# Kernel tuning notes

Hardware: AMD Instinct MI355X
Metric: run time of the kernel (lower is better)

## Reference

```python
import jax, jax.numpy as jnp
import numpy as np

B, IN, OUT = 4096, 1024, 1024


def setup_inputs() -> dict:
    key = jax.random.key(0)
    ks = jax.random.split(key, 11)
    xav = 1.0 / np.sqrt(IN + OUT)  # Xavier-style scale for sigmoid/tanh layers
    d = {
        "x": jax.random.normal(ks[0], (B, IN), dtype=jnp.float32),
        "h": jax.random.normal(ks[1], (B, OUT), dtype=jnp.float32),
        "c": jax.random.normal(ks[2], (B, OUT), dtype=jnp.float32),
        "w_f": jax.random.normal(ks[3], (IN + OUT, OUT), dtype=jnp.float32) * xav,
        "b_f": jnp.zeros((1, OUT), dtype=jnp.float32),
        "w_i": jax.random.normal(ks[4], (IN + OUT, OUT), dtype=jnp.float32) * xav,
        "b_i": jnp.zeros((1, OUT), dtype=jnp.float32),
        "w_c": jax.random.normal(ks[5], (IN + OUT, OUT), dtype=jnp.float32) * xav,
        "b_c": jnp.zeros((1, OUT), dtype=jnp.float32),
        "w_o": jax.random.normal(ks[6], (IN + OUT, OUT), dtype=jnp.float32) * xav,
        "b_o": jnp.zeros((1, OUT), dtype=jnp.float32),
    }
    return d


def reference(x, h, c, w_f, b_f, w_i, b_i, w_c, b_c, w_o, b_o):
    # combined input [B, IN+OUT]
    z = jnp.concatenate([x, h], axis=1)
    f = jax.nn.sigmoid(z @ w_f + b_f)      # forget gate
    i = jax.nn.sigmoid(z @ w_i + b_i)      # update (input) gate
    g = jnp.tanh(z @ w_c + b_c)            # candidate cell
    o = jax.nn.sigmoid(z @ w_o + b_o)      # output gate
    c_new = c * f + i * g
    h_new = jnp.tanh(c_new) * o
    return h_new
```

## Files before the change

### kernel.cpp

```cpp
#include <hip/hip_runtime.h>
#include <hip/hip_bf16.h>

typedef short short8 __attribute__((ext_vector_type(8)));
typedef float f32x4 __attribute__((ext_vector_type(4)));

#define NB 4096
#define KZ 2048
#define NG 1024
#define NKS 32

__device__ __forceinline__ unsigned short f2bf(float f) {
  unsigned int u = __float_as_uint(f);
  u += 0x7FFFu + ((u >> 16) & 1u);
  return (unsigned short)(u >> 16);
}
__device__ __forceinline__ float bf2f(unsigned short s) {
  return __uint_as_float(((unsigned int)s) << 16);
}
__device__ __forceinline__ void gload_lds16(const void* g, void* l) {
  __builtin_amdgcn_global_load_lds(
      (__attribute__((address_space(1))) void*)g,
      (__attribute__((address_space(3))) void*)l, 16, 0, 0);
}
__device__ __forceinline__ float sigm(float x) { return 1.f / (1.f + __expf(-x)); }
__device__ __forceinline__ float tanh_fast(float x) {
  float e = __expf(-2.f * fabsf(x));
  float r = (1.f - e) / (1.f + e);
  return copysignf(r, x);
}

__global__ void zsplit_kernel(const float* __restrict__ x, const float* __restrict__ h,
                              unsigned short* __restrict__ zh) {
  int idx = blockIdx.x * 256 + threadIdx.x;
  int e = idx << 2;
  int r = e >> 11;
  int k = e & (KZ - 1);
  const float* src = (k < 1024) ? (x + ((size_t)r << 10) + k)
                                : (h + ((size_t)r << 10) + (k - 1024));
  float4 v = *reinterpret_cast<const float4*>(src);
  float vf[4] = {v.x, v.y, v.z, v.w};
  unsigned short hh[4];
#pragma unroll
  for (int j = 0; j < 4; ++j) hh[j] = f2bf(vf[j]);
  uint2 H = make_uint2((unsigned)hh[0] | ((unsigned)hh[1] << 16),
                       (unsigned)hh[2] | ((unsigned)hh[3] << 16));
  *reinterpret_cast<uint2*>(zh + e) = H;
}

__global__ void wsplit_kernel(const float* __restrict__ w0, const float* __restrict__ w1,
                              const float* __restrict__ w2, const float* __restrict__ w3,
                              unsigned short* __restrict__ wh, unsigned short* __restrict__ wl) {
  __shared__ float tile[32][33];
  int g = blockIdx.z;
  const float* w = (g == 0) ? w0 : (g == 1) ? w1 : (g == 2) ? w2 : w3;
  int k0 = blockIdx.x << 5;
  int n0 = blockIdx.y << 5;
  int t = threadIdx.x;
  int rk = t >> 3, q = t & 7;
  float4 v = *reinterpret_cast<const float4*>(w + (size_t)(k0 + rk) * NG + n0 + (q << 2));
  tile[rk][(q << 2) + 0] = v.x;
  tile[rk][(q << 2) + 1] = v.y;
  tile[rk][(q << 2) + 2] = v.z;
  tile[rk][(q << 2) + 3] = v.w;
  __syncthreads();
  int n = t >> 3, kq = t & 7;
  unsigned short hs[4], ls[4];
#pragma unroll
  for (int j = 0; j < 4; ++j) {
    float f = tile[(kq << 2) + j][n];
    unsigned short hi = f2bf(f);
    unsigned short lo = f2bf(f - bf2f(hi));
    hs[j] = hi; ls[j] = lo;
  }
  int nn = n0 + n;
  int p = ((nn >> 6) << 8) | (((nn >> 4) & 3) << 6) | (g << 4) | (nn & 15);
  size_t o = (size_t)p * KZ + k0 + (kq << 2);
  uint2 H = make_uint2((unsigned)hs[0] | ((unsigned)hs[1] << 16),
                       (unsigned)hs[2] | ((unsigned)hs[3] << 16));
  uint2 L = make_uint2((unsigned)ls[0] | ((unsigned)ls[1] << 16),
                       (unsigned)ls[2] | ((unsigned)ls[3] << 16));
  *reinterpret_cast<uint2*>(wh + o) = H;
  *reinterpret_cast<uint2*>(wl + o) = L;
}

#define MFMA(a, b, c) __builtin_amdgcn_mfma_f32_16x16x32_bf16((a), (b), (c), 0, 0, 0)
#define ABAR() asm volatile("s_barrier" ::: "memory")
#define LGKM(N) asm volatile("s_waitcnt lgkmcnt(" #N ")" ::: "memory")
#define VMC0() asm volatile("s_waitcnt vmcnt(0)" ::: "memory")
#define SB() __builtin_amdgcn_sched_barrier(0)
#define PRIO1() __builtin_amdgcn_s_setprio(1)
#define PRIO0() __builtin_amdgcn_s_setprio(0)

__global__ __launch_bounds__(512, 2) void lstm_gemm256_kernel(
    const unsigned short* __restrict__ zh,
    const unsigned short* __restrict__ wh, const unsigned short* __restrict__ wl,
    const float* __restrict__ c_in, const float* __restrict__ bf_,
    const float* __restrict__ bi_, const float* __restrict__ bc_,
    const float* __restrict__ bo_, float* __restrict__ out) {
  __shared__ unsigned short As[2 * 16384];
  __shared__ unsigned short Bh[16384];
  __shared__ unsigned short Bl[16384];
  const int t = threadIdx.x;
  const int lane = t & 63;
  const int wid = t >> 6;
  const int wr = wid >> 2;
  const int wc = wid & 3;
  const int l15 = lane & 15;
  const int l4 = lane >> 4;

  const int bid = blockIdx.x;
  const int swz = ((bid & 7) << 5) + (bid >> 3);
  const int bx = swz & 15;
  const int by = swz >> 4;
  const int brow0 = by << 8;
  const int pcol0 = bx << 8;

  char* AsB = (char*)As;
  char* BhB = (char*)Bh;
  char* BlB = (char*)Bl;

  int aoff[2], boff[2];
#pragma unroll
  for (int j = 0; j < 2; ++j) {
    int row = (j << 6) + (t >> 3);
    int sl = (t & 7) ^ (row & 7);
    aoff[j] = (brow0 + row) * KZ + (sl << 3);
    boff[j] = (pcol0 + row) * KZ + (sl << 3);
  }
  const int ldsw = wid << 10;

  auto STAGE = [&](int s, int hx) {
    if (s >= NKS) return;
    const int kk = s << 6;
    if (hx < 2) {
      const int lb = ((s & 1) << 15) + (hx << 14);
#pragma unroll
      for (int j = 0; j < 2; ++j)
        gload_lds16(zh + aoff[j] + hx * (128 * KZ) + kk, AsB + lb + (j << 13) + ldsw);
    } else if (hx < 4) {
      const int hq = hx - 2;
#pragma unroll
      for (int j = 0; j < 2; ++j)
        gload_lds16(wh + boff[j] + hq * (128 * KZ) + kk, BhB + (hq << 14) + (j << 13) + ldsw);
    } else {
      const int hq = hx - 4;
#pragma unroll
      for (int j = 0; j < 2; ++j)
        gload_lds16(wl + boff[j] + hq * (128 * KZ) + kk, BlB + (hq << 14) + (j << 13) + ldsw);
    }
  };

  f32x4 acc[8][4];
#pragma unroll
  for (int m = 0; m < 8; ++m)
#pragma unroll
    for (int n = 0; n < 4; ++n) acc[m][n] = (f32x4){0.f, 0.f, 0.f, 0.f};

  const int rx = l15 & 7;
  const int sx0 = (l4 ^ rx) << 4;
  const int sx1 = ((4 + l4) ^ rx) << 4;
  const int aB = l15 << 7;
  const int bB = ((wc & 1) << 13) + (l15 << 7);
  const int aW = wr << 14;
  const int bW = (wc >> 1) << 14;

  short8 aL0[4], aH0[4], aL1[4], aH1[4], vbh0[4], vbh1[4], vbl0[4], vbl1[4];

  STAGE(0, 0); STAGE(0, 1); STAGE(0, 2); STAGE(0, 3); STAGE(0, 4); STAGE(0, 5);
  VMC0();
  ABAR();

  for (int ks = 0; ks < NKS; ++ks) {
    const int abase = ((ks & 1) << 15) + aW;

#pragma unroll
    for (int m = 0; m < 4; ++m)
      aL0[m] = *reinterpret_cast<const short8*>(AsB + abase + aB + (m << 11) + sx0);
#pragma unroll
    for (int n = 0; n < 4; ++n)
      vbh0[n] = *reinterpret_cast<const short8*>(BhB + bW + bB + (n << 11) + sx0);
    SB();
#pragma unroll
    for (int n = 0; n < 4; ++n)
      vbl0[n] = *reinterpret_cast<const short8*>(BlB + bW + bB + (n << 11) + sx0);
    SB();
    STAGE(ks + 1, 0);
    LGKM(4); SB();
    PRIO1();
#pragma unroll
    for (int m = 0; m < 4; ++m)
#pragma unroll
      for (int n = 0; n < 4; ++n) acc[m][n] = MFMA(aL0[m], vbh0[n], acc[m][n]);
    PRIO0();

#pragma unroll
    for (int m = 0; m < 4; ++m)
      aH0[m] = *reinterpret_cast<const short8*>(AsB + abase + aB + ((m + 4) << 11) + sx0);
    SB();
    STAGE(ks + 1, 1);
    LGKM(4); SB();
    PRIO1();
#pragma unroll
    for (int m = 0; m < 4; ++m)
#pragma unroll
      for (int n = 0; n < 4; ++n) acc[m][n] = MFMA(aL0[m], vbl0[n], acc[m][n]);
    PRIO0();

#pragma unroll
    for (int m = 0; m < 4; ++m)
      aL1[m] = *reinterpret_cast<const short8*>(AsB + abase + aB + (m << 11) + sx1);
#pragma unroll
    for (int n = 0; n < 4; ++n)
      vbh1[n] = *reinterpret_cast<const short8*>(BhB + bW + bB + (n << 11) + sx1);
    SB();
    LGKM(8); SB();
    PRIO1();
#pragma unroll
    for (int m = 0; m < 4; ++m)
#pragma unroll
      for (int n = 0; n < 4; ++n) acc[m + 4][n] = MFMA(aH0[m], vbh0[n], acc[m + 4][n]);
    PRIO0();

#pragma unroll
    for (int n = 0; n < 4; ++n)
      vbl1[n] = *reinterpret_cast<const short8*>(BlB + bW + bB + (n << 11) + sx1);
    SB();
    PRIO1();
#pragma unroll
    for (int m = 0; m < 4; ++m)
#pragma unroll
      for (int n = 0; n < 4; ++n) acc[m + 4][n] = MFMA(aH0[m], vbl0[n], acc[m + 4][n]);
    PRIO0();

    LGKM(0); SB();
    ABAR();
    STAGE(ks + 1, 2); STAGE(ks + 1, 3); STAGE(ks + 1, 4); STAGE(ks + 1, 5);
    PRIO1();
#pragma unroll
    for (int m = 0; m < 4; ++m)
#pragma unroll
      for (int n = 0; n < 4; ++n) acc[m][n] = MFMA(aL1[m], vbh1[n], acc[m][n]);
    PRIO0();

#pragma unroll
    for (int m = 0; m < 4; ++m)
      aH1[m] = *reinterpret_cast<const short8*>(AsB + abase + aB + ((m + 4) << 11) + sx1);
    SB();
    PRIO1();
#pragma unroll
    for (int m = 0; m < 4; ++m)
#pragma unroll
      for (int n = 0; n < 4; ++n) acc[m][n] = MFMA(aL1[m], vbl1[n], acc[m][n]);
    PRIO0();

    LGKM(0); SB();
    PRIO1();
#pragma unroll
    for (int m = 0; m < 4; ++m)
#pragma unroll
      for (int n = 0; n < 4; ++n) acc[m + 4][n] = MFMA(aH1[m], vbh1[n], acc[m + 4][n]);
#pragma unroll
    for (int m = 0; m < 4; ++m)
#pragma unroll
      for (int n = 0; n < 4; ++n) acc[m + 4][n] = MFMA(aH1[m], vbl1[n], acc[m + 4][n]);
    PRIO0();

    VMC0(); SB();
    ABAR();
  }

  const int ng = (bx << 6) + (wc << 4) + l15;
  const float vbf = bf_[ng], vbi = bi_[ng], vbc = bc_[ng], vbo = bo_[ng];
#pragma unroll
  for (int m = 0; m < 8; ++m) {
#pragma unroll
    for (int r = 0; r < 4; ++r) {
      const int row = brow0 + (wr << 7) + (m << 4) + (l4 << 2) + r;
      const float fp = acc[m][0][r] + vbf;
      const float ip = acc[m][1][r] + vbi;
      const float gp = acc[m][2][r] + vbc;
      const float op = acc[m][3][r] + vbo;
      const float co = c_in[(size_t)row * NG + ng];
      const float cnew = co * sigm(fp) + sigm(ip) * tanh_fast(gp);
      out[(size_t)row * NG + ng] = tanh_fast(cnew) * sigm(op);
    }
  }
}

extern "C" void kernel_launch(void* const* d_in, const int* in_sizes, int n_in,
                              void* d_out, int out_size, void* d_ws, size_t ws_size,
                              hipStream_t stream) {
  const float* x   = (const float*)d_in[0];
  const float* h   = (const float*)d_in[1];
  const float* c   = (const float*)d_in[2];
  const float* w_f = (const float*)d_in[3];
  const float* b_f = (const float*)d_in[4];
  const float* w_i = (const float*)d_in[5];
  const float* b_i = (const float*)d_in[6];
  const float* w_c = (const float*)d_in[7];
  const float* b_c = (const float*)d_in[8];
  const float* w_o = (const float*)d_in[9];
  const float* b_o = (const float*)d_in[10];
  float* out = (float*)d_out;

  unsigned short* zh = (unsigned short*)d_ws;
  unsigned short* wh = zh + (size_t)NB * KZ;
  unsigned short* wl = wh + (size_t)KZ * 4096;

  zsplit_kernel<<<(NB * KZ / 4) / 256, 256, 0, stream>>>(x, h, zh);
  wsplit_kernel<<<dim3(KZ / 32, NG / 32, 4), 256, 0, stream>>>(w_f, w_i, w_c, w_o, wh, wl);
  lstm_gemm256_kernel<<<256, 512, 0, stream>>>(zh, wh, wl, c,
                                               b_f, b_i, b_c, b_o, out);
}
```

Before: 131.4 us.

## Load weight fragments directly from global to registers, drop B LDS staging

Removes the LDS buffers for the hi/lo bf16 weight tiles. Each wave now loads its own B fragments straight from global memory into registers with inline global_load_dwordx4, software-pipelined against the MFMA groups through vmcnt waits. The A tile is staged two k-steps ahead into a double-buffered LDS area, and the block-to-tile mapping is changed to an XCD-aware layout. This cuts LDS footprint and traffic, but relies on L2 reuse for the weights and on hand-tuned vmcnt counts, and the MFMA phases now read all eight A fragments at once, which raises register pressure.

Measured after the change: 166.4 us. 26.6% more time.

```diff
diff --git a/kernel.cpp b/kernel.cpp
--- a/kernel.cpp
+++ b/kernel.cpp
@@ -21,6 +21,11 @@
   __builtin_amdgcn_global_load_lds(
       (__attribute__((address_space(1))) void*)g,
       (__attribute__((address_space(3))) void*)l, 16, 0, 0);
+}
+__device__ __forceinline__ short8 bload(const unsigned short* p) {
+  short8 r;
+  asm volatile("global_load_dwordx4 %0, %1, off" : "=v"(r) : "v"(p));
+  return r;
 }
 __device__ __forceinline__ float sigm(float x) { return 1.f / (1.f + __expf(-x)); }
 __device__ __forceinline__ float tanh_fast(float x) {
@@ -84,9 +89,11 @@
 }
 
 #define MFMA(a, b, c) __builtin_amdgcn_mfma_f32_16x16x32_bf16((a), (b), (c), 0, 0, 0)
-#define ABAR() asm volatile("s_barrier" ::: "memory")
-#define LGKM(N) asm volatile("s_waitcnt lgkmcnt(" #N ")" ::: "memory")
+#define BAR() __builtin_amdgcn_s_barrier()
+#define LGKM0() asm volatile("s_waitcnt lgkmcnt(0)" ::: "memory")
 #define VMC0() asm volatile("s_waitcnt vmcnt(0)" ::: "memory")
+#define VMC4() asm volatile("s_waitcnt vmcnt(4)" ::: "memory")
+#define VMC8() asm volatile("s_waitcnt vmcnt(8)" ::: "memory")
 #define SB() __builtin_amdgcn_sched_barrier(0)
 #define PRIO1() __builtin_amdgcn_s_setprio(1)
 #define PRIO0() __builtin_amdgcn_s_setprio(0)
@@ -98,8 +105,6 @@
     const float* __restrict__ bi_, const float* __restrict__ bc_,
     const float* __restrict__ bo_, float* __restrict__ out) {
   __shared__ unsigned short As[2 * 16384];
-  __shared__ unsigned short Bh[16384];
-  __shared__ unsigned short Bl[16384];
   const int t = threadIdx.x;
   const int lane = t & 63;
   const int wid = t >> 6;
@@ -109,45 +114,30 @@
   const int l4 = lane >> 4;
 
   const int bid = blockIdx.x;
-  const int swz = ((bid & 7) << 5) + (bid >> 3);
-  const int bx = swz & 15;
-  const int by = swz >> 4;
+  const int xcd = bid & 7;
+  const int i = bid >> 3;
+  const int bx = (xcd << 1) | (i & 1);
+  const int by = i >> 1;
   const int brow0 = by << 8;
   const int pcol0 = bx << 8;
 
   char* AsB = (char*)As;
-  char* BhB = (char*)Bh;
-  char* BlB = (char*)Bl;
-
-  int aoff[2], boff[2];
-#pragma unroll
-  for (int j = 0; j < 2; ++j) {
+
+  int aoff[4];
+#pragma unroll
+  for (int j = 0; j < 4; ++j) {
     int row = (j << 6) + (t >> 3);
     int sl = (t & 7) ^ (row & 7);
     aoff[j] = (brow0 + row) * KZ + (sl << 3);
-    boff[j] = (pcol0 + row) * KZ + (sl << 3);
   }
   const int ldsw = wid << 10;
 
-  auto STAGE = [&](int s, int hx) {
-    if (s >= NKS) return;
+  auto STAGEA = [&](int s) {
     const int kk = s << 6;
-    if (hx < 2) {
-      const int lb = ((s & 1) << 15) + (hx << 14);
-#pragma unroll
-      for (int j = 0; j < 2; ++j)
-        gload_lds16(zh + aoff[j] + hx * (128 * KZ) + kk, AsB + lb + (j << 13) + ldsw);
-    } else if (hx < 4) {
-      const int hq = hx - 2;
-#pragma unroll
-      for (int j = 0; j < 2; ++j)
-        gload_lds16(wh + boff[j] + hq * (128 * KZ) + kk, BhB + (hq << 14) + (j << 13) + ldsw);
-    } else {
-      const int hq = hx - 4;
-#pragma unroll
-      for (int j = 0; j < 2; ++j)
-        gload_lds16(wl + boff[j] + hq * (128 * KZ) + kk, BlB + (hq << 14) + (j << 13) + ldsw);
-    }
+    const int lb = (s & 1) << 15;
+#pragma unroll
+    for (int j = 0; j < 4; ++j)
+      gload_lds16(zh + aoff[j] + kk, AsB + lb + (j << 13) + ldsw);
   };
 
   f32x4 acc[8][4];
@@ -160,113 +150,81 @@
   const int sx0 = (l4 ^ rx) << 4;
   const int sx1 = ((4 + l4) ^ rx) << 4;
   const int aB = l15 << 7;
-  const int bB = ((wc & 1) << 13) + (l15 << 7);
   const int aW = wr << 14;
-  const int bW = (wc >> 1) << 14;
-
-  short8 aL0[4], aH0[4], aL1[4], aH1[4], vbh0[4], vbh1[4], vbl0[4], vbl1[4];
-
-  STAGE(0, 0); STAGE(0, 1); STAGE(0, 2); STAGE(0, 3); STAGE(0, 4); STAGE(0, 5);
+
+  int rowoff[4];
+#pragma unroll
+  for (int nf = 0; nf < 4; ++nf)
+    rowoff[nf] = (pcol0 + (wc << 6) + (nf << 4) + l15) * KZ;
+  const int kb = l4 << 3;
+
+  short8 a[8], bh0[4], bl0[4], bh1[4], bl1[4];
+
+  STAGEA(0); STAGEA(1);
+#pragma unroll
+  for (int nf = 0; nf < 4; ++nf) bh0[nf] = bload(wh + rowoff[nf] + kb);
   VMC0();
-  ABAR();
-
-  for (int ks = 0; ks < NKS; ++ks) {
-    const int abase = ((ks & 1) << 15) + aW;
-
-#pragma unroll
-    for (int m = 0; m < 4; ++m)
-      aL0[m] = *reinterpret_cast<const short8*>(AsB + abase + aB + (m << 11) + sx0);
-#pragma unroll
-    for (int n = 0; n < 4; ++n)
-      vbh0[n] = *reinterpret_cast<const short8*>(BhB + bW + bB + (n << 11) + sx0);
+  BAR();
+
+  for (int m = 0; m < NKS; ++m) {
+    const int abase = ((m & 1) << 15) + aW;
+    const int kel = m << 6;
+
+#pragma unroll
+    for (int mm = 0; mm < 8; ++mm)
+      a[mm] = *reinterpret_cast<const short8*>(AsB + abase + aB + (mm << 11) + sx0);
+#pragma unroll
+    for (int nf = 0; nf < 4; ++nf) bl0[nf] = bload(wl + rowoff[nf] + kel + kb);
+    if (m < NKS - 1) { VMC8(); } else { VMC4(); }
     SB();
-#pragma unroll
-    for (int n = 0; n < 4; ++n)
-      vbl0[n] = *reinterpret_cast<const short8*>(BlB + bW + bB + (n << 11) + sx0);
+    LGKM0(); SB();
+    PRIO1();
+#pragma unroll
+    for (int mm = 0; mm < 8; ++mm)
+#pragma unroll
+      for (int nf = 0; nf < 4; ++nf) acc[mm][nf] = MFMA(a[mm], bh0[nf], acc[mm][nf]);
+    PRIO0();
+
+#pragma unroll
+    for (int nf = 0; nf < 4; ++nf) bh1[nf] = bload(wh + rowoff[nf] + kel + 32 + kb);
+    VMC4(); SB();
+    PRIO1();
+#pragma unroll
+    for (int mm = 0; mm < 8; ++mm)
+#pragma unroll
+      for (int nf = 0; nf < 4; ++nf) acc[mm][nf] = MFMA(a[mm], bl0[nf], acc[mm][nf]);
+    PRIO0();
+
+#pragma unroll
+    for (int mm = 0; mm < 8; ++mm)
+      a[mm] = *reinterpret_cast<const short8*>(AsB + abase + aB + (mm << 11) + sx1);
+#pragma unroll
+    for (int nf = 0; nf < 4; ++nf) bl1[nf] = bload(wl + rowoff[nf] + kel + 32 + kb);
+    VMC4(); SB();
+    LGKM0(); SB();
+    PRIO1();
+#pragma unroll
+    for (int mm = 0; mm < 8; ++mm)
+#pragma unroll
+      for (int nf = 0; nf < 4; ++nf) acc[mm][nf] = MFMA(a[mm], bh1[nf], acc[mm][nf]);
+    PRIO0();
+
+    BAR();
+    if (m < NKS - 1) {
+#pragma unroll
+      for (int nf = 0; nf < 4; ++nf) bh0[nf] = bload(wh + rowoff[nf] + kel + 64 + kb);
+    }
+    if (m < NKS - 2) STAGEA(m + 2);
+    if (m < NKS - 2)      { VMC8(); }
+    else if (m < NKS - 1) { VMC4(); }
+    else                  { VMC0(); }
     SB();
-    STAGE(ks + 1, 0);
-    LGKM(4); SB();
-    PRIO1();
-#pragma unroll
-    for (int m = 0; m < 4; ++m)
-#pragma unroll
-      for (int n = 0; n < 4; ++n) acc[m][n] = MFMA(aL0[m], vbh0[n], acc[m][n]);
-    PRIO0();
-
-#pragma unroll
-    for (int m = 0; m < 4; ++m)
-      aH0[m] = *reinterpret_cast<const short8*>(AsB + abase + aB + ((m + 4) << 11) + sx0);
-    SB();
-    STAGE(ks + 1, 1);
-    LGKM(4); SB();
-    PRIO1();
-#pragma unroll
-    for (int m = 0; m < 4; ++m)
-#pragma unroll
-      for (int n = 0; n < 4; ++n) acc[m][n] = MFMA(aL0[m], vbl0[n], acc[m][n]);
-    PRIO0();
-
-#pragma unroll
-    for (int m = 0; m < 4; ++m)
-      aL1[m] = *reinterpret_cast<const short8*>(AsB + abase + aB + (m << 11) + sx1);
-#pragma unroll
-    for (int n = 0; n < 4; ++n)
-      vbh1[n] = *reinterpret_cast<const short8*>(BhB + bW + bB + (n << 11) + sx1);
-    SB();
-    LGKM(8); SB();
-    PRIO1();
-#pragma unroll
-    for (int m = 0; m < 4; ++m)
-#pragma unroll
-      for (int n = 0; n < 4; ++n) acc[m + 4][n] = MFMA(aH0[m], vbh0[n], acc[m + 4][n]);
-    PRIO0();
-
-#pragma unroll
-    for (int n = 0; n < 4; ++n)
-      vbl1[n] = *reinterpret_cast<const short8*>(BlB + bW + bB + (n << 11) + sx1);
-    SB();
-    PRIO1();
-#pragma unroll
-    for (int m = 0; m < 4; ++m)
-#pragma unroll
-      for (int n = 0; n < 4; ++n) acc[m + 4][n] = MFMA(aH0[m], vbl0[n], acc[m + 4][n]);
-    PRIO0();
-
-    LGKM(0); SB();
-    ABAR();
-    STAGE(ks + 1, 2); STAGE(ks + 1, 3); STAGE(ks + 1, 4); STAGE(ks + 1, 5);
-    PRIO1();
-#pragma unroll
-    for (int m = 0; m < 4; ++m)
-#pragma unroll
-      for (int n = 0; n < 4; ++n) acc[m][n] = MFMA(aL1[m], vbh1[n], acc[m][n]);
-    PRIO0();
-
-#pragma unroll
-    for (int m = 0; m < 4; ++m)
-      aH1[m] = *reinterpret_cast<const short8*>(AsB + abase + aB + ((m + 4) << 11) + sx1);
-    SB();
-    PRIO1();
-#pragma unroll
-    for (int m = 0; m < 4; ++m)
-#pragma unroll
-      for (int n = 0; n < 4; ++n) acc[m][n] = MFMA(aL1[m], vbl1[n], acc[m][n]);
-    PRIO0();
-
-    LGKM(0); SB();
-    PRIO1();
-#pragma unroll
-    for (int m = 0; m < 4; ++m)
-#pragma unroll
-      for (int n = 0; n < 4; ++n) acc[m + 4][n] = MFMA(aH1[m], vbh1[n], acc[m + 4][n]);
-#pragma unroll
-    for (int m = 0; m < 4; ++m)
-#pragma unroll
-      for (int n = 0; n < 4; ++n) acc[m + 4][n] = MFMA(aH1[m], vbl1[n], acc[m + 4][n]);
-    PRIO0();
-
-    VMC0(); SB();
-    ABAR();
+    PRIO1();
+#pragma unroll
+    for (int mm = 0; mm < 8; ++mm)
+#pragma unroll
+      for (int nf = 0; nf < 4; ++nf) acc[mm][nf] = MFMA(a[mm], bl1[nf], acc[mm][nf]);
+    PRIO0();
   }
 
   const int ng = (bx << 6) + (wc << 4) + l15;
```
